# Performance work log

Hardware: AMD Instinct MI355X
Metric: run time of the kernel (lower is better)

Reference implementation:

```python
import jax, jax.numpy as jnp
import numpy as np

B, C, H, W = 256, 3, 224, 224
IMG_SIZE = 224
BRIGHT, CONTRAST, SAT, HUE = 0.2, 0.2, 0.2, 0.05
P_JITTER, P_CROP = 0.8, 0.5
SCALE_MIN, SCALE_MAX = 0.85, 1.0


def _blend(a, b, ratio):
    # torchvision _blend with float bound 1.0
    return jnp.clip(ratio * a + (1.0 - ratio) * b, 0.0, 1.0)


def _grayscale(x):
    # x: [B,3,H,W] -> [B,H,W]
    return 0.299 * x[:, 0] + 0.587 * x[:, 1] + 0.114 * x[:, 2]


def _adjust_hue(x, hue):
    # x: [B,3,H,W], hue: [B,1,1] offset in [-0.5,0.5]
    r, g, b = x[:, 0], x[:, 1], x[:, 2]
    maxc = jnp.maximum(jnp.maximum(r, g), b)
    minc = jnp.minimum(jnp.minimum(r, g), b)
    v = maxc
    cr = maxc - minc
    eqc = cr == 0.0
    s = cr / jnp.where(eqc, 1.0, maxc)
    crd = jnp.where(eqc, 1.0, cr)
    rc = (maxc - r) / crd
    gc = (maxc - g) / crd
    bc = (maxc - b) / crd
    h = ((maxc == r) * (bc - gc)
         + ((maxc == g) & (maxc != r)) * (2.0 + rc - bc)
         + ((maxc != g) & (maxc != r)) * (4.0 + gc - rc))
    h = jnp.mod(h / 6.0 + 1.0, 1.0)
    h = jnp.mod(h + hue, 1.0)
    # hsv -> rgb
    h6 = h * 6.0
    i = jnp.floor(h6)
    f = h6 - i
    i = i.astype(jnp.int32) % 6
    p = v * (1.0 - s)
    q = v * (1.0 - s * f)
    t = v * (1.0 - s * (1.0 - f))
    m = [(i == k) for k in range(6)]
    r2 = m[0] * v + m[1] * q + m[2] * p + m[3] * p + m[4] * t + m[5] * v
    g2 = m[0] * t + m[1] * v + m[2] * v + m[3] * q + m[4] * p + m[5] * p
    b2 = m[0] * p + m[1] * p + m[2] * t + m[3] * v + m[4] * v + m[5] * q
    return jnp.stack([r2, g2, b2], axis=1)


def _crop_resize_one(im, top, left, ch, cw):
    # im: [C,H,W]; bilinear resize of crop box to IMG_SIZE x IMG_SIZE
    Hh, Ww = im.shape[1], im.shape[2]
    S = IMG_SIZE
    ys = jnp.clip(top + (jnp.arange(S) + 0.5) * ch / S - 0.5, 0.0, Hh - 1.0)
    xs = jnp.clip(left + (jnp.arange(S) + 0.5) * cw / S - 0.5, 0.0, Ww - 1.0)
    y0 = jnp.floor(ys); x0 = jnp.floor(xs)
    wy = (ys - y0)[None, :, None]  # [1,S,1]
    wx = (xs - x0)[None, None, :]  # [1,1,S]
    y0i = y0.astype(jnp.int32); y1i = jnp.minimum(y0i + 1, Hh - 1)
    x0i = x0.astype(jnp.int32); x1i = jnp.minimum(x0i + 1, Ww - 1)
    g = lambda yi, xi: im[:, yi[:, None], xi[None, :]]  # [C,S,S]
    row0 = (1.0 - wx) * g(y0i, x0i) + wx * g(y0i, x1i)
    row1 = (1.0 - wx) * g(y1i, x0i) + wx * g(y1i, x1i)
    return (1.0 - wy) * row0 + wy * row1


def _forward(img, u_jitter, u_bright, u_contrast, u_sat, u_hue, u_crop, u_scale, u_top, u_left):
    # --- color jitter (fixed op order: brightness, contrast, saturation, hue) ---
    bf = (1.0 + (2.0 * u_bright - 1.0) * BRIGHT)[:, None, None, None]
    cf = (1.0 + (2.0 * u_contrast - 1.0) * CONTRAST)[:, None, None, None]
    sf = (1.0 + (2.0 * u_sat - 1.0) * SAT)[:, None, None, None]
    hf = ((2.0 * u_hue - 1.0) * HUE)[:, None, None]
    x = _blend(img, jnp.zeros_like(img), bf)                      # brightness
    mean_gray = _grayscale(x).mean(axis=(-2, -1))[:, None, None, None]
    x = _blend(x, mean_gray, cf)                                  # contrast
    x = _blend(x, _grayscale(x)[:, None], sf)                     # saturation
    x = _adjust_hue(x, hf)                                        # hue
    x = jnp.clip(x, 0.0, 1.0)
    jitter_on = (u_jitter < P_JITTER)[:, None, None, None]
    img = jnp.where(jitter_on, x, img)
    # --- random crop + resize back to IMG_SIZE ---
    Hh, Ww = img.shape[2], img.shape[3]
    scale = SCALE_MIN + (SCALE_MAX - SCALE_MIN) * u_scale
    ch = jnp.floor(Hh * scale)
    cw = jnp.floor(Ww * scale)
    top = jnp.clip(jnp.floor(u_top * (Hh - ch + 1.0)), 0.0, Hh - ch)
    left = jnp.clip(jnp.floor(u_left * (Ww - cw + 1.0)), 0.0, Ww - cw)
    resized = jax.vmap(_crop_resize_one)(img, top, left, ch, cw)
    crop_on = (u_crop < P_CROP)[:, None, None, None]
    return jnp.where(crop_on, resized, img)


def setup_inputs() -> dict:
    key = jax.random.key(0)
    ks = jax.random.split(key, 10)
    names = ['u_jitter', 'u_bright', 'u_contrast', 'u_sat', 'u_hue',
             'u_crop', 'u_scale', 'u_top', 'u_left']
    inp = {'img': jax.random.uniform(ks[0], (B, C, H, W), dtype=jnp.float32)}
    for i, n in enumerate(names):
        inp[n] = jax.random.uniform(ks[i + 1], (B,), dtype=jnp.float32)
    return inp


def reference(img, u_jitter, u_bright, u_contrast, u_sat, u_hue, u_crop, u_scale, u_top, u_left):
    return _forward(img, u_jitter, u_bright, u_contrast, u_sat, u_hue,
                    u_crop, u_scale, u_top, u_left)
```

## Files before the change

kernel.cpp:

```cpp
#include <hip/hip_runtime.h>


static constexpr int   kB     = 256;
static constexpr int   kHW    = 224;
static constexpr int   kNPix  = kHW * kHW;
static constexpr int   kPlane = kNPix;
static constexpr float kPJitter = 0.8f;
static constexpr float kPCrop   = 0.5f;

__device__ __forceinline__ float clamp01(float x) {
    return fminf(fmaxf(x, 0.0f), 1.0f);
}

__device__ __forceinline__ float fast_rcp(float x) {
#if __has_builtin(__builtin_amdgcn_rcpf)
    return __builtin_amdgcn_rcpf(x);
#else
    return 1.0f / x;
#endif
}

struct Px { float r, g, b; };

__device__ __forceinline__ Px jitter_px(Px p, float bf, float cf, float sf,
                                        float hf, float oc) {
    float r = clamp01(bf * p.r);
    float g = clamp01(bf * p.g);
    float b = clamp01(bf * p.b);
    r = clamp01(cf * r + oc);
    g = clamp01(cf * g + oc);
    b = clamp01(cf * b + oc);
    float gray = 0.299f * r + 0.587f * g + 0.114f * b;
    float os = (1.0f - sf) * gray;
    r = clamp01(sf * r + os);
    g = clamp01(sf * g + os);
    b = clamp01(sf * b + os);
    float maxc = fmaxf(fmaxf(r, g), b);
    float minc = fminf(fminf(r, g), b);
    float v  = maxc;
    float cr = maxc - minc;
    bool  eqc = (cr == 0.0f);
    float s   = eqc ? 0.0f : cr * fast_rcp(maxc);
    float inv = eqc ? 1.0f : fast_rcp(cr);
    float rc = (maxc - r) * inv;
    float gc = (maxc - g) * inv;
    float bc = (maxc - b) * inv;
    float h = (maxc == r) ? (bc - gc)
            : (maxc == g) ? (2.0f + rc - bc)
                          : (4.0f + gc - rc);
    h = h * 0.16666667f + 1.0f;
    h = h - floorf(h);
    h = h + hf;
    h = h - floorf(h);
    float h6 = h * 6.0f;
    float fi = floorf(h6);
    float f  = h6 - fi;
    int   i  = ((int)fi) % 6;
    float pp = v * (1.0f - s);
    float qq = v * (1.0f - s * f);
    float tt = v * (1.0f - s * (1.0f - f));
    float r2 = (i == 1) ? qq : ((i == 2) || (i == 3)) ? pp : (i == 4) ? tt : v;
    float g2 = (i == 0) ? tt : ((i == 1) || (i == 2)) ? v  : (i == 3) ? qq : pp;
    float b2 = ((i == 0) || (i == 1)) ? pp : (i == 2) ? tt : (i == 5) ? qq : v;
    Px o;
    o.r = clamp01(r2);
    o.g = clamp01(g2);
    o.b = clamp01(b2);
    return o;
}

__global__ __launch_bounds__(256)
void gray_mean_kernel(const float* __restrict__ img,
                      const float* __restrict__ u_jitter,
                      const float* __restrict__ u_bright,
                      float* __restrict__ gray_sum)
{
    const int b = blockIdx.y;
    if (u_jitter[b] >= kPJitter) return;
    const float bf = 1.0f + (2.0f * u_bright[b] - 1.0f) * 0.2f;
    const float* base = img + (size_t)b * 3 * kPlane;
    const int t = blockIdx.x * 256 + threadIdx.x;
    float acc = 0.0f;
    for (int p = t; p < kNPix; p += 2048) {
        float r  = clamp01(bf * base[p]);
        float g  = clamp01(bf * base[p + kPlane]);
        float bl = clamp01(bf * base[p + 2 * kPlane]);
        acc += 0.299f * r + 0.587f * g + 0.114f * bl;
    }
#pragma unroll
    for (int off = 32; off > 0; off >>= 1)
        acc += __shfl_down(acc, off);
    __shared__ float red[4];
    const int lane = threadIdx.x & 63;
    const int w    = threadIdx.x >> 6;
    if (lane == 0) red[w] = acc;
    __syncthreads();
    if (threadIdx.x == 0)
        atomicAdd(&gray_sum[b], red[0] + red[1] + red[2] + red[3]);
}

__global__ __launch_bounds__(256)
void aug_main_kernel(const float* __restrict__ img,
                     const float* __restrict__ u_jitter,
                     const float* __restrict__ u_bright,
                     const float* __restrict__ u_contrast,
                     const float* __restrict__ u_sat,
                     const float* __restrict__ u_hue,
                     const float* __restrict__ u_crop,
                     const float* __restrict__ u_scale,
                     const float* __restrict__ u_top,
                     const float* __restrict__ u_left,
                     const float* __restrict__ gray_sum,
                     float* __restrict__ out)
{
    const int b   = blockIdx.y;
    const int pix = blockIdx.x * 256 + threadIdx.x;
    const int oy  = pix / kHW;
    const int ox  = pix - oy * kHW;

    const bool jitter_on = u_jitter[b] < kPJitter;
    const bool crop_on   = u_crop[b]   < kPCrop;

    float bf = 1.0f, cf = 1.0f, sf = 1.0f, hf = 0.0f, oc = 0.0f;
    if (jitter_on) {
        bf = 1.0f + (2.0f * u_bright[b]   - 1.0f) * 0.2f;
        cf = 1.0f + (2.0f * u_contrast[b] - 1.0f) * 0.2f;
        sf = 1.0f + (2.0f * u_sat[b]      - 1.0f) * 0.2f;
        hf = (2.0f * u_hue[b] - 1.0f) * 0.05f;
        const float mg = gray_sum[b] * (1.0f / (float)kNPix);
        oc = (1.0f - cf) * mg;
    }

    const float* base = img + (size_t)b * 3 * kPlane;
    float outr, outg, outb;

    if (crop_on) {
        float top, left, ch;
        {
#pragma clang fp contract(off)
            float scale = 0.85f + 0.15f * u_scale[b];
            ch = floorf(224.0f * scale);
            float rem = (224.0f - ch) + 1.0f;
            top  = fminf(fmaxf(floorf(u_top[b]  * rem), 0.0f), 224.0f - ch);
            left = fminf(fmaxf(floorf(u_left[b] * rem), 0.0f), 224.0f - ch);
        }
        float fy, fx;
        {
#pragma clang fp contract(off)
            fy = top  + ((float)oy + 0.5f) * ch / 224.0f - 0.5f;
            fx = left + ((float)ox + 0.5f) * ch / 224.0f - 0.5f;
        }
        fy = fminf(fmaxf(fy, 0.0f), 223.0f);
        fx = fminf(fmaxf(fx, 0.0f), 223.0f);
        float y0f = floorf(fy), x0f = floorf(fx);
        float wy = fy - y0f,   wx = fx - x0f;
        int y0 = (int)y0f, x0 = (int)x0f;
        int y1 = min(y0 + 1, kHW - 1), x1 = min(x0 + 1, kHW - 1);

        int idx[4] = { y0 * kHW + x0, y0 * kHW + x1,
                       y1 * kHW + x0, y1 * kHW + x1 };
        Px px[4];
#pragma unroll
        for (int j = 0; j < 4; ++j) {
            Px p;
            p.r = base[idx[j]];
            p.g = base[idx[j] + kPlane];
            p.b = base[idx[j] + 2 * kPlane];
            px[j] = jitter_on ? jitter_px(p, bf, cf, sf, hf, oc) : p;
        }
        float r0 = (1.0f - wx) * px[0].r + wx * px[1].r;
        float r1 = (1.0f - wx) * px[2].r + wx * px[3].r;
        outr = (1.0f - wy) * r0 + wy * r1;
        float g0 = (1.0f - wx) * px[0].g + wx * px[1].g;
        float g1 = (1.0f - wx) * px[2].g + wx * px[3].g;
        outg = (1.0f - wy) * g0 + wy * g1;
        float b0 = (1.0f - wx) * px[0].b + wx * px[1].b;
        float b1 = (1.0f - wx) * px[2].b + wx * px[3].b;
        outb = (1.0f - wy) * b0 + wy * b1;
    } else {
        const int idx = oy * kHW + ox;
        Px p;
        p.r = base[idx];
        p.g = base[idx + kPlane];
        p.b = base[idx + 2 * kPlane];
        if (jitter_on) p = jitter_px(p, bf, cf, sf, hf, oc);
        outr = p.r; outg = p.g; outb = p.b;
    }

    const size_t o = (size_t)b * 3 * kPlane + (size_t)oy * kHW + ox;
    out[o]              = outr;
    out[o + kPlane]     = outg;
    out[o + 2 * kPlane] = outb;
}

extern "C" void kernel_launch(void* const* d_in, const int* in_sizes, int n_in,
                              void* d_out, int out_size, void* d_ws, size_t ws_size,
                              hipStream_t stream) {
    const float* img = (const float*)d_in[0];
    const float* uj  = (const float*)d_in[1];
    const float* ub  = (const float*)d_in[2];
    const float* uc  = (const float*)d_in[3];
    const float* us  = (const float*)d_in[4];
    const float* uh  = (const float*)d_in[5];
    const float* ucr = (const float*)d_in[6];
    const float* usc = (const float*)d_in[7];
    const float* ut  = (const float*)d_in[8];
    const float* ul  = (const float*)d_in[9];
    float* gray_sum  = (float*)d_ws;
    float* out       = (float*)d_out;

    hipMemsetAsync(gray_sum, 0, kB * sizeof(float), stream);

    dim3 gridA(8, kB, 1);
    gray_mean_kernel<<<gridA, 256, 0, stream>>>(img, uj, ub, gray_sum);

    dim3 gridB(kNPix / 256, kB, 1);
    aug_main_kernel<<<gridB, 256, 0, stream>>>(img, uj, ub, uc, us, uh,
                                               ucr, usc, ut, ul, gray_sum, out);
}
```

Before: 335.7 us.

## Stage jittered source rows in LDS for crop-resize and vectorize non-crop path

The main kernel now handles four output rows per block. In the crop path it loads a 5-row source band, applies the colour jitter once per source pixel into shared memory, and then does the bilinear interpolation from LDS, so jitter is no longer recomputed for each of the four taps. The non-crop path uses float4 loads and stores. The gray-mean kernel becomes one 1024-thread block per image with float4 loads and a direct store, which removes the memset and the atomics. The 5-row band assumes the crop scale is at least 0.85 so four output rows span at most five source rows, and the non-crop path leaves 32 of 256 threads idle.

Result: faster. 308.2 us (-8.2%).

```diff
diff --git a/kernel.cpp b/kernel.cpp
--- a/kernel.cpp
+++ b/kernel.cpp
@@ -1,12 +1,11 @@
 #include <hip/hip_runtime.h>
 
 
-static constexpr int   kB     = 256;
-static constexpr int   kHW    = 224;
-static constexpr int   kNPix  = kHW * kHW;
-static constexpr int   kPlane = kNPix;
-static constexpr float kPJitter = 0.8f;
-static constexpr float kPCrop   = 0.5f;
+static constexpr int   kB      = 256;
+static constexpr int   kHW     = 224;
+static constexpr int   kNPix   = kHW * kHW;
+static constexpr int   kPlane  = kNPix;
+static constexpr int   kPlane4 = kNPix / 4;
 
 __device__ __forceinline__ float clamp01(float x) {
     return fminf(fmaxf(x, 0.0f), 1.0f);
@@ -69,34 +68,40 @@
     return o;
 }
 
-__global__ __launch_bounds__(256)
+__global__ __launch_bounds__(1024)
 void gray_mean_kernel(const float* __restrict__ img,
                       const float* __restrict__ u_jitter,
                       const float* __restrict__ u_bright,
                       float* __restrict__ gray_sum)
 {
-    const int b = blockIdx.y;
-    if (u_jitter[b] >= kPJitter) return;
+    const int b = blockIdx.x;
+    if (u_jitter[b] >= 0.8f) return;
     const float bf = 1.0f + (2.0f * u_bright[b] - 1.0f) * 0.2f;
-    const float* base = img + (size_t)b * 3 * kPlane;
-    const int t = blockIdx.x * 256 + threadIdx.x;
+    const float4* pr = (const float4*)(img + (size_t)b * 3 * kPlane);
+    const float4* pg = pr + kPlane4;
+    const float4* pb = pr + 2 * kPlane4;
     float acc = 0.0f;
-    for (int p = t; p < kNPix; p += 2048) {
-        float r  = clamp01(bf * base[p]);
-        float g  = clamp01(bf * base[p + kPlane]);
-        float bl = clamp01(bf * base[p + 2 * kPlane]);
-        acc += 0.299f * r + 0.587f * g + 0.114f * bl;
+    for (int i = threadIdx.x; i < kPlane4; i += 1024) {
+        float4 r = pr[i], g = pg[i], bl = pb[i];
+        acc += 0.299f * clamp01(bf * r.x) + 0.587f * clamp01(bf * g.x) + 0.114f * clamp01(bf * bl.x);
+        acc += 0.299f * clamp01(bf * r.y) + 0.587f * clamp01(bf * g.y) + 0.114f * clamp01(bf * bl.y);
+        acc += 0.299f * clamp01(bf * r.z) + 0.587f * clamp01(bf * g.z) + 0.114f * clamp01(bf * bl.z);
+        acc += 0.299f * clamp01(bf * r.w) + 0.587f * clamp01(bf * g.w) + 0.114f * clamp01(bf * bl.w);
     }
 #pragma unroll
     for (int off = 32; off > 0; off >>= 1)
         acc += __shfl_down(acc, off);
-    __shared__ float red[4];
+    __shared__ float red[16];
     const int lane = threadIdx.x & 63;
     const int w    = threadIdx.x >> 6;
     if (lane == 0) red[w] = acc;
     __syncthreads();
-    if (threadIdx.x == 0)
-        atomicAdd(&gray_sum[b], red[0] + red[1] + red[2] + red[3]);
+    if (threadIdx.x == 0) {
+        float s = 0.0f;
+#pragma unroll
+        for (int k = 0; k < 16; ++k) s += red[k];
+        gray_sum[b] = s;
+    }
 }
 
 __global__ __launch_bounds__(256)
@@ -114,12 +119,11 @@
                      float* __restrict__ out)
 {
     const int b   = blockIdx.y;
-    const int pix = blockIdx.x * 256 + threadIdx.x;
-    const int oy  = pix / kHW;
-    const int ox  = pix - oy * kHW;
-
-    const bool jitter_on = u_jitter[b] < kPJitter;
-    const bool crop_on   = u_crop[b]   < kPCrop;
+    const int oy0 = blockIdx.x * 4;
+    const int t   = threadIdx.x;
+
+    const bool jitter_on = u_jitter[b] < 0.8f;
+    const bool crop_on   = u_crop[b]   < 0.5f;
 
     float bf = 1.0f, cf = 1.0f, sf = 1.0f, hf = 0.0f, oc = 0.0f;
     if (jitter_on) {
@@ -131,19 +135,73 @@
         oc = (1.0f - cf) * mg;
     }
 
-    const float* base = img + (size_t)b * 3 * kPlane;
-    float outr, outg, outb;
-
-    if (crop_on) {
-        float top, left, ch;
-        {
+    const float* base  = img + (size_t)b * 3 * kPlane;
+    float*       obase = out + (size_t)b * 3 * kPlane;
+
+    if (!crop_on) {
+        if (t < 224) {
+            const int f4 = oy0 * (kHW / 4) + t;
+            const float4* p4 = (const float4*)base;
+            float4 r4 = p4[f4];
+            float4 g4 = p4[f4 + kPlane4];
+            float4 b4 = p4[f4 + 2 * kPlane4];
+            if (jitter_on) {
+                Px a0 = jitter_px({r4.x, g4.x, b4.x}, bf, cf, sf, hf, oc);
+                Px a1 = jitter_px({r4.y, g4.y, b4.y}, bf, cf, sf, hf, oc);
+                Px a2 = jitter_px({r4.z, g4.z, b4.z}, bf, cf, sf, hf, oc);
+                Px a3 = jitter_px({r4.w, g4.w, b4.w}, bf, cf, sf, hf, oc);
+                r4 = {a0.r, a1.r, a2.r, a3.r};
+                g4 = {a0.g, a1.g, a2.g, a3.g};
+                b4 = {a0.b, a1.b, a2.b, a3.b};
+            }
+            float4* o4 = (float4*)obase;
+            o4[f4]               = r4;
+            o4[f4 + kPlane4]     = g4;
+            o4[f4 + 2 * kPlane4] = b4;
+        }
+        return;
+    }
+
+    float ch, top, left;
+    {
 #pragma clang fp contract(off)
-            float scale = 0.85f + 0.15f * u_scale[b];
-            ch = floorf(224.0f * scale);
-            float rem = (224.0f - ch) + 1.0f;
-            top  = fminf(fmaxf(floorf(u_top[b]  * rem), 0.0f), 224.0f - ch);
-            left = fminf(fmaxf(floorf(u_left[b] * rem), 0.0f), 224.0f - ch);
-        }
+        float scale = 0.85f + 0.15f * u_scale[b];
+        ch = floorf(224.0f * scale);
+        float rem = (224.0f - ch) + 1.0f;
+        top  = fminf(fmaxf(floorf(u_top[b]  * rem), 0.0f), 224.0f - ch);
+        left = fminf(fmaxf(floorf(u_left[b] * rem), 0.0f), 224.0f - ch);
+    }
+
+    int ybase;
+    {
+#pragma clang fp contract(off)
+        float fy0 = top + ((float)oy0 + 0.5f) * ch / 224.0f - 0.5f;
+        fy0 = fminf(fmaxf(fy0, 0.0f), 223.0f);
+        ybase = (int)floorf(fy0);
+    }
+    ybase = min(ybase, kHW - 5);
+
+    __shared__ float sm[3][5 * kHW];
+
+    for (int p = t; p < 5 * kHW; p += 256) {
+        const int r   = p / kHW;
+        const int col = p - r * kHW;
+        const int gi  = (ybase + r) * kHW + col;
+        Px q;
+        q.r = base[gi];
+        q.g = base[gi + kPlane];
+        q.b = base[gi + 2 * kPlane];
+        if (jitter_on) q = jitter_px(q, bf, cf, sf, hf, oc);
+        sm[0][p] = q.r;
+        sm[1][p] = q.g;
+        sm[2][p] = q.b;
+    }
+    __syncthreads();
+
+    for (int o = t; o < 4 * kHW; o += 256) {
+        const int dy = o / kHW;
+        const int ox = o - dy * kHW;
+        const int oy = oy0 + dy;
         float fy, fx;
         {
 #pragma clang fp contract(off)
@@ -152,45 +210,24 @@
         }
         fy = fminf(fmaxf(fy, 0.0f), 223.0f);
         fx = fminf(fmaxf(fx, 0.0f), 223.0f);
-        float y0f = floorf(fy), x0f = floorf(fx);
-        float wy = fy - y0f,   wx = fx - x0f;
-        int y0 = (int)y0f, x0 = (int)x0f;
-        int y1 = min(y0 + 1, kHW - 1), x1 = min(x0 + 1, kHW - 1);
-
-        int idx[4] = { y0 * kHW + x0, y0 * kHW + x1,
-                       y1 * kHW + x0, y1 * kHW + x1 };
-        Px px[4];
+        const float y0f = floorf(fy), x0f = floorf(fx);
+        const float wy = fy - y0f,    wx = fx - x0f;
+        const int y0 = (int)y0f, x0 = (int)x0f;
+        const int y1 = min(y0 + 1, kHW - 1), x1 = min(x0 + 1, kHW - 1);
+        const int r0 = (y0 - ybase) * kHW;
+        const int r1 = (y1 - ybase) * kHW;
+        const int oo = oy * kHW + ox;
 #pragma unroll
-        for (int j = 0; j < 4; ++j) {
-            Px p;
-            p.r = base[idx[j]];
-            p.g = base[idx[j] + kPlane];
-            p.b = base[idx[j] + 2 * kPlane];
-            px[j] = jitter_on ? jitter_px(p, bf, cf, sf, hf, oc) : p;
+        for (int c = 0; c < 3; ++c) {
+            const float v00 = sm[c][r0 + x0];
+            const float v01 = sm[c][r0 + x1];
+            const float v10 = sm[c][r1 + x0];
+            const float v11 = sm[c][r1 + x1];
+            const float a0 = (1.0f - wx) * v00 + wx * v01;
+            const float a1 = (1.0f - wx) * v10 + wx * v11;
+            obase[c * kPlane + oo] = (1.0f - wy) * a0 + wy * a1;
         }
-        float r0 = (1.0f - wx) * px[0].r + wx * px[1].r;
-        float r1 = (1.0f - wx) * px[2].r + wx * px[3].r;
-        outr = (1.0f - wy) * r0 + wy * r1;
-        float g0 = (1.0f - wx) * px[0].g + wx * px[1].g;
-        float g1 = (1.0f - wx) * px[2].g + wx * px[3].g;
-        outg = (1.0f - wy) * g0 + wy * g1;
-        float b0 = (1.0f - wx) * px[0].b + wx * px[1].b;
-        float b1 = (1.0f - wx) * px[2].b + wx * px[3].b;
-        outb = (1.0f - wy) * b0 + wy * b1;
-    } else {
-        const int idx = oy * kHW + ox;
-        Px p;
-        p.r = base[idx];
-        p.g = base[idx + kPlane];
-        p.b = base[idx + 2 * kPlane];
-        if (jitter_on) p = jitter_px(p, bf, cf, sf, hf, oc);
-        outr = p.r; outg = p.g; outb = p.b;
-    }
-
-    const size_t o = (size_t)b * 3 * kPlane + (size_t)oy * kHW + ox;
-    out[o]              = outr;
-    out[o + kPlane]     = outg;
-    out[o + 2 * kPlane] = outb;
+    }
 }
 
 extern "C" void kernel_launch(void* const* d_in, const int* in_sizes, int n_in,
@@ -209,12 +246,9 @@
     float* gray_sum  = (float*)d_ws;
     float* out       = (float*)d_out;
 
-    hipMemsetAsync(gray_sum, 0, kB * sizeof(float), stream);
-
-    dim3 gridA(8, kB, 1);
-    gray_mean_kernel<<<gridA, 256, 0, stream>>>(img, uj, ub, gray_sum);
-
-    dim3 gridB(kNPix / 256, kB, 1);
+    gray_mean_kernel<<<dim3(kB), 1024, 0, stream>>>(img, uj, ub, gray_sum);
+
+    dim3 gridB(kHW / 4, kB, 1);
     aug_main_kernel<<<gridB, 256, 0, stream>>>(img, uj, ub, uc, us, uh,
                                                ucr, usc, ut, ul, gray_sum, out);
 }
```
